# Kernel optimization log

Measured on AMD Instinct MI355X. Metric: run time of the kernel, lower is better.

## Reference

```python
import jax, jax.numpy as jnp
import numpy as np

D_MODEL = 1024
N_HEADS = 16
N_KV = 4
HEAD_DIM = D_MODEL // N_HEADS  # 64
EPS = 1e-5
THETA = 10000.0


def _rope_tables(S):
    half = HEAD_DIM // 2
    inv_freq = 1.0 / (THETA ** (jnp.arange(half, dtype=jnp.float32) / half))
    t = jnp.arange(S, dtype=jnp.float32)
    f = t[:, None] * inv_freq[None, :]  # [S, half]
    return jnp.cos(f), jnp.sin(f)


def _apply_rope(x, cos, sin):
    # x: [B, H, S, D]
    half = x.shape[-1] // 2
    x1, x2 = x[..., :half], x[..., half:]
    c = cos[None, None, :, :]
    s = sin[None, None, :, :]
    return jnp.concatenate([x1 * c - x2 * s, x1 * s + x2 * c], axis=-1)


def _rmsnorm(x, scale):
    rms = jnp.sqrt(jnp.mean(x * x, axis=-1, keepdims=True) + EPS)
    return x / rms * scale


def setup_inputs() -> dict:
    key = jax.random.key(0)
    ks = jax.random.split(key, 4)
    B, S = 2, 2048
    x = jax.random.normal(ks[0], (B, S, D_MODEL), dtype=jnp.float32)
    Wq = jax.random.normal(ks[1], (D_MODEL, D_MODEL), dtype=jnp.float32) * 0.02
    Wkv = jax.random.normal(ks[2], (D_MODEL, 2 * N_KV * HEAD_DIM), dtype=jnp.float32) * 0.02
    Wo = jax.random.normal(ks[3], (D_MODEL, D_MODEL), dtype=jnp.float32) * 0.02
    q_scale = jnp.ones((HEAD_DIM,), dtype=jnp.float32)
    k_scale = jnp.ones((HEAD_DIM,), dtype=jnp.float32)
    return {"x": x, "Wq": Wq, "Wkv": Wkv, "Wo": Wo,
            "q_scale": q_scale, "k_scale": k_scale}


def reference(x, Wq, Wkv, Wo, q_scale, k_scale):
    B, S, D = x.shape
    groups = N_HEADS // N_KV  # GQA group size

    # projections
    q = (x @ Wq).reshape(B, S, N_HEADS, HEAD_DIM).transpose(0, 2, 1, 3)  # [B,H,S,d]
    kv = x @ Wkv
    k, v = jnp.split(kv, 2, axis=-1)
    k = k.reshape(B, S, N_KV, HEAD_DIM).transpose(0, 2, 1, 3)  # [B,Hkv,S,d]
    v = v.reshape(B, S, N_KV, HEAD_DIM).transpose(0, 2, 1, 3)

    # per-head QK-RMSNorm (before RoPE, as in the torch module)
    q = _rmsnorm(q, q_scale)
    k = _rmsnorm(k, k_scale)

    # RoPE
    cos, sin = _rope_tables(S)
    q = _apply_rope(q, cos, sin)
    k = _apply_rope(k, cos, sin)

    # causal GQA attention (equivalent to SDPA with enable_gqa=True)
    qg = q.reshape(B, N_KV, groups, S, HEAD_DIM)
    scale = 1.0 / np.sqrt(HEAD_DIM).astype(np.float32)
    scores = jnp.einsum('bkgsd,bktd->bkgst', qg, k) * scale  # [B,Hkv,g,S,S]
    causal = jnp.tril(jnp.ones((S, S), dtype=bool))
    scores = jnp.where(causal[None, None, None], scores, -jnp.inf)
    attn = jax.nn.softmax(scores, axis=-1)
    out = jnp.einsum('bkgst,bktd->bkgsd', attn, v)
    out = out.reshape(B, N_HEADS, S, HEAD_DIM).transpose(0, 2, 1, 3).reshape(B, S, D)
    return out @ Wo
```

## Files before the change

### kernel.cpp

```cpp
#include <hip/hip_runtime.h>

#define S_LEN 2048
#define BATCH 2
#define DM    1024
#define NH    16
#define NKV   4
#define HD    64
#define MROWS (BATCH * S_LEN)
#define NQKV  1536

typedef __attribute__((ext_vector_type(8))) short bf16x8;
typedef __attribute__((ext_vector_type(4))) short s16x4;
typedef __attribute__((ext_vector_type(4))) float f32x4;
typedef __attribute__((ext_vector_type(4))) int i32x4;

__device__ __forceinline__ unsigned short f2bf(float f) {
  unsigned int u = __float_as_uint(f);
  u += 0x7FFF + ((u >> 16) & 1);
  return (unsigned short)(u >> 16);
}

__device__ __forceinline__ void gload_lds16(const unsigned short* g, unsigned short* l) {
  __builtin_amdgcn_global_load_lds((const __attribute__((address_space(1))) void*)g,
                                   (__attribute__((address_space(3))) void*)l, 16, 0, 0);
}
__device__ __forceinline__ void gload_lds4(const unsigned short* g, unsigned short* l) {
  __builtin_amdgcn_global_load_lds((const __attribute__((address_space(1))) void*)g,
                                   (__attribute__((address_space(3))) void*)l, 4, 0, 0);
}

__global__ __launch_bounds__(256) void prep_kernel(const float* __restrict__ x,
                                                   unsigned short* __restrict__ xb,
                                                   const float* __restrict__ Wq,
                                                   const float* __restrict__ Wkv,
                                                   const float* __restrict__ Wo,
                                                   unsigned short* __restrict__ wt1,
                                                   unsigned short* __restrict__ wot) {
  __shared__ float tile[64][65];
  int bid = blockIdx.x;
  int t = threadIdx.x;
  if (bid < 4096) {
    int i = (bid * 256 + t) * 4;
    float4 v = *reinterpret_cast<const float4*>(x + i);
    xb[i + 0] = f2bf(v.x);
    xb[i + 1] = f2bf(v.y);
    xb[i + 2] = f2bf(v.z);
    xb[i + 3] = f2bf(v.w);
    return;
  }
  bid -= 4096;
  const float* in;
  unsigned short* out;
  int C, bx, by;
  if (bid < 256) { in = Wq; out = wt1; C = 1024; bx = bid & 15; by = bid >> 4; }
  else if (bid < 384) { int k = bid - 256; in = Wkv; out = wt1 + 1024 * 1024; C = 512; bx = k & 7; by = k >> 3; }
  else { int k = bid - 384; in = Wo; out = wot; C = 1024; bx = k & 15; by = k >> 4; }
  const int R = 1024;
  int r0 = by * 64, c0 = bx * 64;
  int rl = t >> 2, cs = (t & 3) * 16;
#pragma unroll
  for (int k = 0; k < 4; ++k) {
    float4 v = *reinterpret_cast<const float4*>(in + (size_t)(r0 + rl) * C + c0 + cs + 4 * k);
    tile[rl][cs + 4 * k + 0] = v.x;
    tile[rl][cs + 4 * k + 1] = v.y;
    tile[rl][cs + 4 * k + 2] = v.z;
    tile[rl][cs + 4 * k + 3] = v.w;
  }
  __syncthreads();
  int cl = t >> 2, rs = (t & 3) * 16;
  bf16x8 v0, v1;
#pragma unroll
  for (int i = 0; i < 8; ++i) v0[i] = (short)f2bf(tile[rs + i][cl]);
#pragma unroll
  for (int i = 0; i < 8; ++i) v1[i] = (short)f2bf(tile[rs + 8 + i][cl]);
  unsigned short* dst = out + (size_t)(c0 + cl) * R + r0 + rs;
  *reinterpret_cast<bf16x8*>(dst) = v0;
  *reinterpret_cast<bf16x8*>(dst + 8) = v1;
}

__global__ __launch_bounds__(256) void gemm1_fused(const unsigned short* __restrict__ A,
                                                   const unsigned short* __restrict__ BT,
                                                   const float* __restrict__ q_scale,
                                                   const float* __restrict__ k_scale,
                                                   unsigned short* __restrict__ qb,
                                                   unsigned short* __restrict__ kbuf,
                                                   unsigned short* __restrict__ vt,
                                                   int K) {
  __shared__ __align__(16) unsigned short As[128 * 64];
  __shared__ __align__(16) unsigned short Bs[64 * 64];
  int bx = blockIdx.x;
  int row0 = blockIdx.y * 128, col0 = bx * 64;
  int t = threadIdx.x;
  int w = t >> 6, lane = t & 63, quad = lane >> 4, l16 = lane & 15;
  int srow = lane >> 3;
  int scol = (lane & 7) * 8;

  f32x4 acc[2][4];
#pragma unroll
  for (int i = 0; i < 2; ++i)
#pragma unroll
    for (int j = 0; j < 4; ++j) acc[i][j] = (f32x4){0.f, 0.f, 0.f, 0.f};

  for (int k0 = 0; k0 < K; k0 += 64) {
#pragma unroll
    for (int j = 0; j < 4; ++j)
      gload_lds16(A + (size_t)(row0 + w * 32 + j * 8 + srow) * K + k0 + scol,
                  &As[(w * 32 + j * 8) * 64]);
#pragma unroll
    for (int j = 0; j < 2; ++j)
      gload_lds16(BT + (size_t)(col0 + w * 16 + j * 8 + srow) * K + k0 + scol,
                  &Bs[(w * 16 + j * 8) * 64]);
    __syncthreads();
#pragma unroll
    for (int ks = 0; ks < 2; ++ks) {
      bf16x8 af[2], bfr[4];
#pragma unroll
      for (int i = 0; i < 2; ++i)
        af[i] = *reinterpret_cast<const bf16x8*>(&As[(w * 32 + i * 16 + l16) * 64 + ks * 32 + quad * 8]);
#pragma unroll
      for (int j = 0; j < 4; ++j)
        bfr[j] = *reinterpret_cast<const bf16x8*>(&Bs[(j * 16 + l16) * 64 + ks * 32 + quad * 8]);
#pragma unroll
      for (int i = 0; i < 2; ++i)
#pragma unroll
        for (int j = 0; j < 4; ++j)
          acc[i][j] = __builtin_amdgcn_mfma_f32_16x16x32_bf16(af[i], bfr[j], acc[i][j], 0, 0, 0);
    }
    __syncthreads();
  }

  if (bx < 20) {
    const float* scale = (bx < 16) ? q_scale : k_scale;
    float post = (bx < 16) ? 1.0f : 0.125f * 1.44269504088896f;
    float sc0 = scale[l16], sc1 = scale[16 + l16], sc2 = scale[32 + l16], sc3 = scale[48 + l16];
    float invf0 = exp2f((float)l16 * (-13.2877123795495f / 32.0f));
    float invf1 = exp2f((float)(l16 + 16) * (-13.2877123795495f / 32.0f));
#pragma unroll
    for (int i = 0; i < 2; ++i)
#pragma unroll
      for (int rg = 0; rg < 4; ++rg) {
        int row = row0 + w * 32 + i * 16 + quad * 4 + rg;
        int b = row >> 11, s = row & 2047;
        float v0 = acc[i][0][rg], v1 = acc[i][1][rg], v2 = acc[i][2][rg], v3 = acc[i][3][rg];
        float ss = v0 * v0 + v1 * v1 + v2 * v2 + v3 * v3;
        ss += __shfl_xor(ss, 1, 64);
        ss += __shfl_xor(ss, 2, 64);
        ss += __shfl_xor(ss, 4, 64);
        ss += __shfl_xor(ss, 8, 64);
        float inv_rms = 1.0f / sqrtf(ss * (1.0f / 64.0f) + 1e-5f);
        float n0 = v0 * inv_rms * sc0, n1 = v1 * inv_rms * sc1;
        float n2 = v2 * inv_rms * sc2, n3 = v3 * inv_rms * sc3;
        float f0 = (float)s * invf0, f1 = (float)s * invf1;
        float c0 = __cosf(f0), s0 = __sinf(f0), c1 = __cosf(f1), s1 = __sinf(f1);
        float o0 = (n0 * c0 - n2 * s0) * post;
        float o1 = (n1 * c1 - n3 * s1) * post;
        float o2 = (n0 * s0 + n2 * c0) * post;
        float o3 = (n1 * s1 + n3 * c1) * post;
        unsigned short* dst = (bx < 16)
            ? qb + ((size_t)(b * NH + bx) * S_LEN + s) * HD
            : kbuf + ((size_t)(b * NKV + (bx - 16)) * S_LEN + s) * HD;
        dst[l16] = f2bf(o0);
        dst[16 + l16] = f2bf(o1);
        dst[32 + l16] = f2bf(o2);
        dst[48 + l16] = f2bf(o3);
      }
  } else {
    int kvh = bx - 20;
    int b = row0 >> 11;
    unsigned short* vbase = vt + (size_t)(b * NKV + kvh) * HD * S_LEN;
#pragma unroll
    for (int i = 0; i < 2; ++i) {
      int s0 = (row0 & 2047) + w * 32 + i * 16 + quad * 4;
#pragma unroll
      for (int j = 0; j < 4; ++j) {
        int d = j * 16 + l16;
        s16x4 pv;
#pragma unroll
        for (int rg = 0; rg < 4; ++rg) pv[rg] = (short)f2bf(acc[i][j][rg]);
        *reinterpret_cast<s16x4*>(vbase + (size_t)d * S_LEN + s0) = pv;
      }
    }
  }
}

#define CH 136
#define TILE_SH (32 * CH)
__global__ __launch_bounds__(256, 4) void attn_kernel(const unsigned short* __restrict__ qb,
                                                      const unsigned short* __restrict__ kbuf,
                                                      const unsigned short* __restrict__ vt,
                                                      unsigned short* __restrict__ Opart,
                                                      float* __restrict__ lpart) {
  __shared__ __align__(16) unsigned short Ks[2][TILE_SH];
  __shared__ __align__(16) unsigned short Vs[2][TILE_SH];
  const size_t OZ = (size_t)BATCH * NH * S_LEN * HD;
  const size_t LZ = (size_t)BATCH * NH * S_LEN;
  int t32 = 63 - (int)(blockIdx.x >> 4);
  int sub = blockIdx.x & 15;
  int z = sub & 1;
  int bkv = sub >> 1;
  int b = bkv >> 2, kvh = bkv & 3;
  int w = threadIdx.x >> 6;
  int h = kvh * 4 + w;
  int lane = threadIdx.x & 63;
  int quad = lane >> 4, l16 = lane & 15;
  int qa = t32 * 32 + l16;
  const unsigned short* Q = qb + (size_t)(b * NH + h) * S_LEN * HD;
  const unsigned short* Kh = kbuf + (size_t)(b * NKV + kvh) * S_LEN * HD;
  const unsigned short* Vh = vt + (size_t)(b * NKV + kvh) * HD * S_LEN;

  bf16x8 bqa0 = *reinterpret_cast<const bf16x8*>(Q + (size_t)qa * HD + quad * 8);
  bf16x8 bqa1 = *reinterpret_cast<const bf16x8*>(Q + (size_t)qa * HD + 32 + quad * 8);
  bf16x8 bqb0 = *reinterpret_cast<const bf16x8*>(Q + (size_t)(qa + 16) * HD + quad * 8);
  bf16x8 bqb1 = *reinterpret_cast<const bf16x8*>(Q + (size_t)(qa + 16) * HD + 32 + quad * 8);

  bf16x8 ones;
#pragma unroll
  for (int i = 0; i < 8; ++i) ones[i] = (short)0x3F80;

  f32x4 ot[2][4];
#pragma unroll
  for (int gq = 0; gq < 2; ++gq)
#pragma unroll
    for (int i = 0; i < 4; ++i) ot[gq][i] = (f32x4){0.f, 0.f, 0.f, 0.f};
  f32x4 ol[2] = {(f32x4){0.f, 0.f, 0.f, 0.f}, (f32x4){0.f, 0.f, 0.f, 0.f}};

  int n = (t32 >> 1) + 1;

  auto stage = [&](int kbase, int dbuf) {
    const unsigned short* kg = Kh + (size_t)(kbase + w * 16) * HD + lane * 2;
    const unsigned short* vg = Vh + (size_t)(w * 16 + (lane >> 5)) * S_LEN + kbase + (lane & 31) * 2;
    unsigned short* kl = &Ks[dbuf][(w * 8) * CH];
    unsigned short* vl = &Vs[dbuf][(w * 8) * CH];
#pragma unroll
    for (int c = 0; c < 8; ++c) {
      gload_lds4(kg + (size_t)(2 * c) * HD, kl + c * CH);
      gload_lds4(vg + (size_t)(2 * c) * S_LEN, vl + c * CH);
    }
  };

  if (z < n) {
    stage(z << 6, 0);
    __syncthreads();

    for (int kb = z; kb < n; kb += 2) {
      int dbuf = (kb >> 1) & 1;
      bool diag = (kb == n - 1);
      if (kb + 2 < n) stage((kb + 2) << 6, dbuf ^ 1);
      int kbase = kb << 6;
      const unsigned short* Kd = Ks[dbuf];
      const unsigned short* Vd = Vs[dbuf];

      f32x4 sa[4], sb[4];
      __builtin_amdgcn_s_setprio(1);
#pragma unroll
      for (int km = 0; km < 4; ++km) {
        int kk = 32 * (km >> 1) + 4 * (km & 1) + 8 * (l16 >> 2) + (l16 & 3);
        int base = (kk >> 1) * CH + (kk & 1) * 64;
        bf16x8 k0 = *reinterpret_cast<const bf16x8*>(&Kd[base + quad * 8]);
        bf16x8 k1 = *reinterpret_cast<const bf16x8*>(&Kd[base + 32 + quad * 8]);
        f32x4 s = {0.f, 0.f, 0.f, 0.f};
        s = __builtin_amdgcn_mfma_f32_16x16x32_bf16(k0, bqa0, s, 0, 0, 0);
        s = __builtin_amdgcn_mfma_f32_16x16x32_bf16(k1, bqa1, s, 0, 0, 0);
        sa[km] = s;
        f32x4 s2 = {0.f, 0.f, 0.f, 0.f};
        s2 = __builtin_amdgcn_mfma_f32_16x16x32_bf16(k0, bqb0, s2, 0, 0, 0);
        s2 = __builtin_amdgcn_mfma_f32_16x16x32_bf16(k1, bqb1, s2, 0, 0, 0);
        sb[km] = s2;
      }
      __builtin_amdgcn_s_setprio(0);
      if (diag) {
#pragma unroll
        for (int km = 0; km < 4; ++km)
#pragma unroll
          for (int rg = 0; rg < 4; ++rg) {
            int key = kbase + 32 * (km >> 1) + 8 * quad + 4 * (km & 1) + rg;
            if (key > qa) sa[km][rg] = -1e30f;
            if (key > qa + 16) sb[km][rg] = -1e30f;
          }
      }
      unsigned int pk[4][2], qk[4][2];
#pragma unroll
      for (int km = 0; km < 4; ++km) {
        float a0 = exp2f(sa[km][0]), a1 = exp2f(sa[km][1]);
        float a2 = exp2f(sa[km][2]), a3 = exp2f(sa[km][3]);
        pk[km][0] = __builtin_amdgcn_perm(__float_as_uint(a1), __float_as_uint(a0), 0x07060302);
        pk[km][1] = __builtin_amdgcn_perm(__float_as_uint(a3), __float_as_uint(a2), 0x07060302);
        float b0 = exp2f(sb[km][0]), b1 = exp2f(sb[km][1]);
        float b2 = exp2f(sb[km][2]), b3 = exp2f(sb[km][3]);
        qk[km][0] = __builtin_amdgcn_perm(__float_as_uint(b1), __float_as_uint(b0), 0x07060302);
        qk[km][1] = __builtin_amdgcn_perm(__float_as_uint(b3), __float_as_uint(b2), 0x07060302);
      }
      i32x4 wa0 = {(int)pk[0][0], (int)pk[0][1], (int)pk[1][0], (int)pk[1][1]};
      i32x4 wa1 = {(int)pk[2][0], (int)pk[2][1], (int)pk[3][0], (int)pk[3][1]};
      i32x4 wb0 = {(int)qk[0][0], (int)qk[0][1], (int)qk[1][0], (int)qk[1][1]};
      i32x4 wb1 = {(int)qk[2][0], (int)qk[2][1], (int)qk[3][0], (int)qk[3][1]};
      bf16x8 pa0 = *reinterpret_cast<bf16x8*>(&wa0);
      bf16x8 pa1 = *reinterpret_cast<bf16x8*>(&wa1);
      bf16x8 pb0 = *reinterpret_cast<bf16x8*>(&wb0);
      bf16x8 pb1 = *reinterpret_cast<bf16x8*>(&wb1);
      __builtin_amdgcn_s_setprio(1);
      ol[0] = __builtin_amdgcn_mfma_f32_16x16x32_bf16(ones, pa0, ol[0], 0, 0, 0);
      ol[0] = __builtin_amdgcn_mfma_f32_16x16x32_bf16(ones, pa1, ol[0], 0, 0, 0);
      ol[1] = __builtin_amdgcn_mfma_f32_16x16x32_bf16(ones, pb0, ol[1], 0, 0, 0);
      ol[1] = __builtin_amdgcn_mfma_f32_16x16x32_bf16(ones, pb1, ol[1], 0, 0, 0);
#pragma unroll
      for (int dm = 0; dm < 4; ++dm) {
        int ch = dm * 8 + (l16 >> 1);
        int base = ch * CH + (l16 & 1) * 64;
        bf16x8 v0 = *reinterpret_cast<const bf16x8*>(&Vd[base + quad * 8]);
        bf16x8 v1 = *reinterpret_cast<const bf16x8*>(&Vd[base + 32 + quad * 8]);
        ot[0][dm] = __builtin_amdgcn_mfma_f32_16x16x32_bf16(v0, pa0, ot[0][dm], 0, 0, 0);
        ot[0][dm] = __builtin_amdgcn_mfma_f32_16x16x32_bf16(v1, pa1, ot[0][dm], 0, 0, 0);
        ot[1][dm] = __builtin_amdgcn_mfma_f32_16x16x32_bf16(v0, pb0, ot[1][dm], 0, 0, 0);
        ot[1][dm] = __builtin_amdgcn_mfma_f32_16x16x32_bf16(v1, pb1, ot[1][dm], 0, 0, 0);
      }
      __builtin_amdgcn_s_setprio(0);
      __syncthreads();
    }
  }

  unsigned short* Oz = Opart + (size_t)z * OZ;
  float* lz = lpart + (size_t)z * LZ;
#pragma unroll
  for (int gq = 0; gq < 2; ++gq) {
    size_t base = ((size_t)(b * NH + h) * S_LEN + qa + gq * 16) * HD;
#pragma unroll
    for (int dm = 0; dm < 4; ++dm) {
      s16x4 pv;
#pragma unroll
      for (int rg = 0; rg < 4; ++rg) pv[rg] = (short)f2bf(ot[gq][dm][rg]);
      *reinterpret_cast<s16x4*>(Oz + base + dm * 16 + quad * 4) = pv;
    }
  }
  if (quad == 0) {
    size_t lb = (size_t)(b * NH + h) * S_LEN + t32 * 32 + l16;
    lz[lb] = ol[0][0];
    lz[lb + 16] = ol[1][0];
  }
}

__global__ __launch_bounds__(256) void attn_combine_kernel(const unsigned short* __restrict__ Opart,
                                                           const float* __restrict__ lpart,
                                                           unsigned short* __restrict__ ctx) {
  const size_t OZ = (size_t)BATCH * NH * S_LEN * HD;
  const size_t LZ = (size_t)BATCH * NH * S_LEN;
  int i8 = blockIdx.x * 256 + threadIdx.x;
  size_t i = (size_t)i8 * 8;
  int row = i8 >> 3;
  bf16x8 a = *reinterpret_cast<const bf16x8*>(Opart + i);
  bf16x8 c = *reinterpret_cast<const bf16x8*>(Opart + OZ + i);
  float inv = 1.0f / (lpart[row] + lpart[LZ + row]);
  int q = row & 2047;
  int bh = row >> 11;
  int b = bh >> 4, h = bh & 15;
  int d0 = (i8 & 7) * 8;
  bf16x8 o;
#pragma unroll
  for (int k = 0; k < 8; ++k) {
    float fa = __uint_as_float(((unsigned int)(unsigned short)a[k]) << 16);
    float fc = __uint_as_float(((unsigned int)(unsigned short)c[k]) << 16);
    o[k] = (short)f2bf((fa + fc) * inv);
  }
  *reinterpret_cast<bf16x8*>(ctx + ((size_t)(b * S_LEN + q)) * DM + h * HD + d0) = o;
}

__global__ __launch_bounds__(256) void gemm_bt_n64(const unsigned short* __restrict__ A,
                                                   const unsigned short* __restrict__ BT,
                                                   float* __restrict__ C,
                                                   int M, int N, int K) {
  __shared__ __align__(16) unsigned short As[128 * 64];
  __shared__ __align__(16) unsigned short Bs[64 * 64];
  int row0 = blockIdx.y * 128, col0 = blockIdx.x * 64;
  int t = threadIdx.x;
  int w = t >> 6, lane = t & 63, quad = lane >> 4, l16 = lane & 15;
  int srow = lane >> 3;
  int scol = (lane & 7) * 8;

  f32x4 acc[2][4];
#pragma unroll
  for (int i = 0; i < 2; ++i)
#pragma unroll
    for (int j = 0; j < 4; ++j) acc[i][j] = (f32x4){0.f, 0.f, 0.f, 0.f};

  for (int k0 = 0; k0 < K; k0 += 64) {
#pragma unroll
    for (int j = 0; j < 4; ++j)
      gload_lds16(A + (size_t)(row0 + w * 32 + j * 8 + srow) * K + k0 + scol,
                  &As[(w * 32 + j * 8) * 64]);
#pragma unroll
    for (int j = 0; j < 2; ++j)
      gload_lds16(BT + (size_t)(col0 + w * 16 + j * 8 + srow) * K + k0 + scol,
                  &Bs[(w * 16 + j * 8) * 64]);
    __syncthreads();
#pragma unroll
    for (int ks = 0; ks < 2; ++ks) {
      bf16x8 af[2], bfr[4];
#pragma unroll
      for (int i = 0; i < 2; ++i)
        af[i] = *reinterpret_cast<const bf16x8*>(&As[(w * 32 + i * 16 + l16) * 64 + ks * 32 + quad * 8]);
#pragma unroll
      for (int j = 0; j < 4; ++j)
        bfr[j] = *reinterpret_cast<const bf16x8*>(&Bs[(j * 16 + l16) * 64 + ks * 32 + quad * 8]);
#pragma unroll
      for (int i = 0; i < 2; ++i)
#pragma unroll
        for (int j = 0; j < 4; ++j)
          acc[i][j] = __builtin_amdgcn_mfma_f32_16x16x32_bf16(af[i], bfr[j], acc[i][j], 0, 0, 0);
    }
    __syncthreads();
  }
#pragma unroll
  for (int i = 0; i < 2; ++i)
#pragma unroll
    for (int j = 0; j < 4; ++j) {
      int row = row0 + w * 32 + i * 16 + quad * 4;
      float* Cptr = C + (size_t)row * N + col0 + j * 16 + l16;
#pragma unroll
      for (int rg = 0; rg < 4; ++rg) Cptr[(size_t)rg * N] = acc[i][j][rg];
    }
}

extern "C" void kernel_launch(void* const* d_in, const int* in_sizes, int n_in,
                              void* d_out, int out_size, void* d_ws, size_t ws_size,
                              hipStream_t stream) {
  const float* x = (const float*)d_in[0];
  const float* Wq = (const float*)d_in[1];
  const float* Wkv = (const float*)d_in[2];
  const float* Wo = (const float*)d_in[3];
  const float* q_scale = (const float*)d_in[4];
  const float* k_scale = (const float*)d_in[5];
  float* out = (float*)d_out;

  char* ws = (char*)d_ws;
  size_t off = 0;
  auto alloc = [&](size_t bytes) {
    void* p = ws + off;
    off += (bytes + 255) & ~(size_t)255;
    return p;
  };
  unsigned short* xb = (unsigned short*)alloc((size_t)MROWS * DM * 2);
  unsigned short* wt1 = (unsigned short*)alloc((size_t)NQKV * DM * 2);
  unsigned short* wot = (unsigned short*)alloc((size_t)DM * DM * 2);
  unsigned short* qb = (unsigned short*)alloc((size_t)BATCH * NH * S_LEN * HD * 2);
  unsigned short* kbuf = (unsigned short*)alloc((size_t)BATCH * NKV * S_LEN * HD * 2);
  unsigned short* vt = (unsigned short*)alloc((size_t)BATCH * NKV * HD * S_LEN * 2);
  unsigned short* ctx = (unsigned short*)alloc((size_t)MROWS * DM * 2);
  unsigned short* Opart = (unsigned short*)alloc(2 * (size_t)BATCH * NH * S_LEN * HD * 2);
  float* lpart = (float*)alloc(2 * (size_t)BATCH * NH * S_LEN * 4);

  prep_kernel<<<4736, 256, 0, stream>>>(x, xb, Wq, Wkv, Wo, wt1, wot);

  gemm1_fused<<<dim3(NQKV / 64, MROWS / 128), 256, 0, stream>>>(xb, wt1, q_scale, k_scale,
                                                                qb, kbuf, vt, DM);

  attn_kernel<<<1024, 256, 0, stream>>>(qb, kbuf, vt, Opart, lpart);
  attn_combine_kernel<<<(BATCH * NH * S_LEN * HD / 8) / 256, 256, 0, stream>>>(Opart, lpart, ctx);

  gemm_bt_n64<<<dim3(DM / 64, MROWS / 128), 256, 0, stream>>>(ctx, wot, out, MROWS, DM, DM);
}
```

Before: 171.1 us.

## Fuse split-KV attention combine into the output projection GEMM A-tile load

Removes the separate combine kernel and the ctx buffer. The output-projection GEMM now reads both attention partials and their row sums directly, normalizes them and converts to bf16 in registers, then stores the A tile into LDS with an XOR swizzle to avoid bank conflicts. This saves one kernel launch and a full write and read of ctx. In exchange, each of the 16 column blocks repeats the combine arithmetic and reads twice as many partial bytes, and the A load becomes synchronous instead of an async global-to-LDS copy.

```diff
diff --git a/kernel.cpp b/kernel.cpp
--- a/kernel.cpp
+++ b/kernel.cpp
@@ -339,35 +339,13 @@
   }
 }
 
-__global__ __launch_bounds__(256) void attn_combine_kernel(const unsigned short* __restrict__ Opart,
-                                                           const float* __restrict__ lpart,
-                                                           unsigned short* __restrict__ ctx) {
+__global__ __launch_bounds__(256) void gemm2_fused(const unsigned short* __restrict__ Opart,
+                                                   const float* __restrict__ lpart,
+                                                   const unsigned short* __restrict__ BT,
+                                                   float* __restrict__ C) {
   const size_t OZ = (size_t)BATCH * NH * S_LEN * HD;
   const size_t LZ = (size_t)BATCH * NH * S_LEN;
-  int i8 = blockIdx.x * 256 + threadIdx.x;
-  size_t i = (size_t)i8 * 8;
-  int row = i8 >> 3;
-  bf16x8 a = *reinterpret_cast<const bf16x8*>(Opart + i);
-  bf16x8 c = *reinterpret_cast<const bf16x8*>(Opart + OZ + i);
-  float inv = 1.0f / (lpart[row] + lpart[LZ + row]);
-  int q = row & 2047;
-  int bh = row >> 11;
-  int b = bh >> 4, h = bh & 15;
-  int d0 = (i8 & 7) * 8;
-  bf16x8 o;
-#pragma unroll
-  for (int k = 0; k < 8; ++k) {
-    float fa = __uint_as_float(((unsigned int)(unsigned short)a[k]) << 16);
-    float fc = __uint_as_float(((unsigned int)(unsigned short)c[k]) << 16);
-    o[k] = (short)f2bf((fa + fc) * inv);
-  }
-  *reinterpret_cast<bf16x8*>(ctx + ((size_t)(b * S_LEN + q)) * DM + h * HD + d0) = o;
-}
-
-__global__ __launch_bounds__(256) void gemm_bt_n64(const unsigned short* __restrict__ A,
-                                                   const unsigned short* __restrict__ BT,
-                                                   float* __restrict__ C,
-                                                   int M, int N, int K) {
+  const int N = DM, K = DM;
   __shared__ __align__(16) unsigned short As[128 * 64];
   __shared__ __align__(16) unsigned short Bs[64 * 64];
   int row0 = blockIdx.y * 128, col0 = blockIdx.x * 64;
@@ -383,21 +361,40 @@
     for (int j = 0; j < 4; ++j) acc[i][j] = (f32x4){0.f, 0.f, 0.f, 0.f};
 
   for (int k0 = 0; k0 < K; k0 += 64) {
-#pragma unroll
-    for (int j = 0; j < 4; ++j)
-      gload_lds16(A + (size_t)(row0 + w * 32 + j * 8 + srow) * K + k0 + scol,
-                  &As[(w * 32 + j * 8) * 64]);
+    int h = k0 >> 6;
 #pragma unroll
     for (int j = 0; j < 2; ++j)
       gload_lds16(BT + (size_t)(col0 + w * 16 + j * 8 + srow) * K + k0 + scol,
                   &Bs[(w * 16 + j * 8) * 64]);
+#pragma unroll
+    for (int j = 0; j < 4; ++j) {
+      int r = row0 + w * 32 + j * 8 + srow;
+      int b = r >> 11, q = r & 2047;
+      size_t orow = (size_t)(b * NH + h) * S_LEN + q;
+      size_t off = orow * HD + scol;
+      bf16x8 a0 = *reinterpret_cast<const bf16x8*>(Opart + off);
+      bf16x8 a1 = *reinterpret_cast<const bf16x8*>(Opart + OZ + off);
+      float inv = 1.0f / (lpart[orow] + lpart[LZ + orow]);
+      bf16x8 o;
+#pragma unroll
+      for (int k = 0; k < 8; ++k) {
+        float fa = __uint_as_float(((unsigned int)(unsigned short)a0[k]) << 16);
+        float fc = __uint_as_float(((unsigned int)(unsigned short)a1[k]) << 16);
+        o[k] = (short)f2bf((fa + fc) * inv);
+      }
+      int colu = (scol >> 3) ^ srow;
+      *reinterpret_cast<bf16x8*>(&As[(w * 32 + j * 8 + srow) * 64 + (colu << 3)]) = o;
+    }
     __syncthreads();
 #pragma unroll
     for (int ks = 0; ks < 2; ++ks) {
       bf16x8 af[2], bfr[4];
 #pragma unroll
-      for (int i = 0; i < 2; ++i)
-        af[i] = *reinterpret_cast<const bf16x8*>(&As[(w * 32 + i * 16 + l16) * 64 + ks * 32 + quad * 8]);
+      for (int i = 0; i < 2; ++i) {
+        int arow = w * 32 + i * 16 + l16;
+        int colu = (ks * 4 + quad) ^ (l16 & 7);
+        af[i] = *reinterpret_cast<const bf16x8*>(&As[arow * 64 + (colu << 3)]);
+      }
 #pragma unroll
       for (int j = 0; j < 4; ++j)
         bfr[j] = *reinterpret_cast<const bf16x8*>(&Bs[(j * 16 + l16) * 64 + ks * 32 + quad * 8]);
@@ -444,7 +441,6 @@
   unsigned short* qb = (unsigned short*)alloc((size_t)BATCH * NH * S_LEN * HD * 2);
   unsigned short* kbuf = (unsigned short*)alloc((size_t)BATCH * NKV * S_LEN * HD * 2);
   unsigned short* vt = (unsigned short*)alloc((size_t)BATCH * NKV * HD * S_LEN * 2);
-  unsigned short* ctx = (unsigned short*)alloc((size_t)MROWS * DM * 2);
   unsigned short* Opart = (unsigned short*)alloc(2 * (size_t)BATCH * NH * S_LEN * HD * 2);
   float* lpart = (float*)alloc(2 * (size_t)BATCH * NH * S_LEN * 4);
 
@@ -454,7 +450,6 @@
                                                                 qb, kbuf, vt, DM);
 
   attn_kernel<<<1024, 256, 0, stream>>>(qb, kbuf, vt, Opart, lpart);
-  attn_combine_kernel<<<(BATCH * NH * S_LEN * HD / 8) / 256, 256, 0, stream>>>(Opart, lpart, ctx);
-
-  gemm_bt_n64<<<dim3(DM / 64, MROWS / 128), 256, 0, stream>>>(ctx, wot, out, MROWS, DM, DM);
-}
+
+  gemm2_fused<<<dim3(DM / 64, MROWS / 128), 256, 0, stream>>>(Opart, lpart, wot, out);
+}
```

Measured after the change: 188.7 us. +10.3%, slower.
